# Kernel optimization log

Hardware: AMD Instinct MI355X
Metric: run time of the kernel (lower is better)

The kernel has to match this reference:

```python
import jax, jax.numpy as jnp
import numpy as np

WS, OWS, NH, C = 16, 24, 6, 192


def setup_inputs() -> dict:
    key = jax.random.key(0)
    ks = jax.random.split(key, 20)
    s = 0.05
    inp = {
        'x': jax.random.normal(ks[0], (2, C, 128, 128), jnp.float32),
        'depth': jax.random.normal(ks[1], (2, C, 128, 128), jnp.float32),
        'rpi': jax.random.randint(ks[2], (WS * WS, OWS * OWS), 0, (WS + OWS - 1) ** 2),
        'norm1_w': jnp.ones((C,), jnp.float32),
        'norm1_b': jnp.zeros((C,), jnp.float32),
        'qkv_w': jax.random.normal(ks[3], (C, 3 * C), jnp.float32) * s,
        'qkv_b': jax.random.normal(ks[4], (3 * C,), jnp.float32) * s,
        'dproj_w': jax.random.normal(ks[5], (C, C), jnp.float32) * s,
        'dproj_b': jax.random.normal(ks[6], (C,), jnp.float32) * s,
        'rpb_table': jax.random.normal(ks[7], ((WS + OWS - 1) ** 2, NH), jnp.float32) * 0.02,
        'proj_w': jax.random.normal(ks[8], (C, C), jnp.float32) * s,
        'proj_b': jax.random.normal(ks[9], (C,), jnp.float32) * s,
        'norm2_w': jnp.ones((C,), jnp.float32),
        'norm2_b': jnp.zeros((C,), jnp.float32),
        'fc1_w': jax.random.normal(ks[10], (C, 2 * C), jnp.float32) * s,
        'fc1_b': jax.random.normal(ks[11], (2 * C,), jnp.float32) * s,
        'fc2_w': jax.random.normal(ks[12], (2 * C, C), jnp.float32) * s,
        'fc2_b': jax.random.normal(ks[13], (C,), jnp.float32) * s,
    }
    return inp


def _ln(t, g, b):
    mu = t.mean(-1, keepdims=True)
    var = ((t - mu) ** 2).mean(-1, keepdims=True)
    return (t - mu) / jnp.sqrt(var + 1e-5) * g + b


def reference(x, depth, rpi, norm1_w, norm1_b, qkv_w, qkv_b, dproj_w, dproj_b,
              rpb_table, proj_w, proj_b, norm2_w, norm2_b, fc1_w, fc1_b, fc2_w, fc2_b):
    b, c, h, w = x.shape
    d = c // NH
    scale = d ** -0.5
    pad = (OWS - WS) // 2
    nh, nw = h // WS, w // WS

    xf = jnp.transpose(x, (0, 2, 3, 1))  # b h w c
    qkv = _ln(xf, norm1_w, norm1_b) @ qkv_w + qkv_b  # b h w 3c
    k, v = qkv[..., c:2 * c], qkv[..., 2 * c:]
    # depth_proj is a 1x1 conv == per-pixel linear
    q = jnp.einsum('bhwi,oi->bhwo', jnp.transpose(depth, (0, 2, 3, 1)), dproj_w) + dproj_b

    # non-overlapping query windows
    qw = q.reshape(b, nh, WS, nw, WS, c).transpose(0, 1, 3, 2, 4, 5).reshape(-1, WS * WS, c)

    # overlapping KV windows (unfold: kernel OWS, stride WS, pad (OWS-WS)//2)
    kv = jnp.concatenate([k, v], axis=-1)  # b h w 2c
    kvp = jnp.pad(kv, ((0, 0), (pad, pad), (pad, pad), (0, 0)))
    hh = (jnp.arange(nh) * WS)[:, None] + jnp.arange(OWS)[None]  # [nh, OWS]
    ww = (jnp.arange(nw) * WS)[:, None] + jnp.arange(OWS)[None]  # [nw, OWS]
    patches = kvp[:, hh[:, None, :, None], ww[None, :, None, :], :]  # b nh nw OWS OWS 2c
    patches = patches.reshape(-1, OWS * OWS, 2 * c)
    kw, vw = patches[..., :c], patches[..., c:]

    B, nq, n = qw.shape[0], WS * WS, OWS * OWS
    qh = qw.reshape(B, nq, NH, d).transpose(0, 2, 1, 3) * scale
    kh = kw.reshape(B, n, NH, d).transpose(0, 2, 1, 3)
    vh = vw.reshape(B, n, NH, d).transpose(0, 2, 1, 3)

    attn = jnp.einsum('bhqd,bhkd->bhqk', qh, kh)
    bias = rpb_table[rpi.reshape(-1)].reshape(nq, n, NH).transpose(2, 0, 1)  # H nq n
    attn = jax.nn.softmax(attn + bias[None], axis=-1)
    out = jnp.einsum('bhqk,bhkd->bhqd', attn, vh).transpose(0, 2, 1, 3).reshape(B, nq, c)

    out = out.reshape(b, nh, nw, WS, WS, c).transpose(0, 1, 3, 2, 4, 5).reshape(b, h, w, c)
    out = out @ proj_w + proj_b + xf  # residual
    y = out + (jax.nn.gelu(_ln(out, norm2_w, norm2_b) @ fc1_w + fc1_b, approximate=False) @ fc2_w + fc2_b)
    return jnp.transpose(y, (0, 3, 1, 2))
```

## Files before the change

### kernel.cpp

```cpp
#include <hip/hip_runtime.h>
#include <math.h>

typedef __attribute__((ext_vector_type(8))) short s16x8;
typedef __attribute__((ext_vector_type(4))) short s16x4;
typedef __attribute__((ext_vector_type(4))) float f32x4;

#define DEV __device__ __forceinline__

DEV float b2f(unsigned short u){ unsigned int x = ((unsigned int)u)<<16u; return __builtin_bit_cast(float,x); }
DEV unsigned short f2b(float f){
  unsigned int x = __builtin_bit_cast(unsigned int,f);
  x += 0x7fffu + ((x>>16)&1u);
  return (unsigned short)(x>>16);
}
DEV unsigned int pk_bf16(float lo, float hi){
  unsigned int r;
  asm("v_cvt_pk_bf16_f32 %0, %1, %2" : "=v"(r) : "v"(lo), "v"(hi));
  return r;
}
DEV float ex2(float x){
  float r;
  asm("v_exp_f32 %0, %1" : "=v"(r) : "v"(x));
  return r;
}
DEV float rcpf(float x){
  float r;
  asm("v_rcp_f32 %0, %1" : "=v"(r) : "v"(x));
  return r;
}
#define LOG2E 1.4426950408889634f

__global__ __launch_bounds__(256) void prep_all(
    const float* __restrict__ x, const float* __restrict__ depth,
    const float* __restrict__ g, const float* __restrict__ be,
    const float* __restrict__ qkvw, const float* __restrict__ dprojw,
    const float* __restrict__ projw, const float* __restrict__ fc1w,
    const float* __restrict__ fc2w, const int* __restrict__ rpi,
    const float* __restrict__ rpb,
    unsigned short* xn, unsigned short* xf, unsigned short* dn,
    unsigned short* kvw, unsigned short* dpw, unsigned short* pjw,
    unsigned short* f1w, unsigned short* f2w, unsigned short* bt){
  __shared__ float t[64][193];
  __shared__ float ps[4][64], pq[4][64];
  __shared__ float mu_s[64], rs_s[64];
  int tid = threadIdx.x;
  int bid = blockIdx.x;
  if(bid >= 512){
    int i = (bid - 512)*256 + tid;
    if(i < 73728){
      int n = i/192, k = i - n*192;
      kvw[i] = f2b(qkvw[k*576 + 192 + n]);
    } else if(i < 110592){
      int j = i - 73728;
      dpw[j] = f2b(dprojw[j]);
    } else if(i < 147456){
      int j = i - 110592; int n = j/192, k = j - n*192;
      pjw[j] = f2b(projw[k*192 + n]);
    } else if(i < 221184){
      int j = i - 147456; int n = j/192, k = j - n*192;
      f1w[j] = f2b(fc1w[k*384 + n]);
    } else if(i < 294912){
      int j = i - 221184; int n = j/384, k = j - n*384;
      f2w[j] = f2b(fc2w[k*192 + n]);
    } else {
      int j = i - 294912;
      int h = j/147456; int rr = j - h*147456;
      int kk = rr >> 8; int q = rr & 255;
      int step = kk >> 5, within = kk & 31;
      int lg = within >> 3, p4r = within & 7;
      bt[h*147456 + step*8192 + lg*2048 + q*8 + p4r] =
          f2b(rpb[rpi[q*576 + kk]*6 + h] * LOG2E);
    }
    return;
  }
  long tokbase = (long)bid * 64;
  int b = (int)(tokbase >> 14); int hw = (int)(tokbase & 16383);
  const float* xb = x + ((long)b*192)*16384 + hw;
  int tok = tid & 63, cpart = tid >> 6;
  for(int c = cpart; c < 192; c += 4) t[tok][c] = xb[(long)c*16384 + tok];
  __syncthreads();
  float s = 0.f, q = 0.f;
  #pragma unroll 4
  for(int i = 0; i < 48; i++){ float v = t[tok][cpart*48 + i]; s += v; q += v*v; }
  ps[cpart][tok] = s; pq[cpart][tok] = q;
  __syncthreads();
  if(tid < 64){
    float ss = ps[0][tid]+ps[1][tid]+ps[2][tid]+ps[3][tid];
    float qq = pq[0][tid]+pq[1][tid]+pq[2][tid]+pq[3][tid];
    float mu = ss * (1.f/192.f);
    float var = qq * (1.f/192.f) - mu*mu;
    mu_s[tid] = mu; rs_s[tid] = 1.f/sqrtf(var + 1e-5f);
  }
  __syncthreads();
  long obase = tokbase * 192;
  for(int u = tid; u < 64*192; u += 256){
    int tk = u / 192, ch = u - tk*192;
    float v = t[tk][ch];
    xf[obase + u] = f2b(v);
    xn[obase + u] = f2b((v - mu_s[tk]) * rs_s[tk] * g[ch] + be[ch]);
  }
  __syncthreads();
  const float* db = depth + ((long)b*192)*16384 + hw;
  for(int c = cpart; c < 192; c += 4) t[tok][c] = db[(long)c*16384 + tok];
  __syncthreads();
  for(int u = tid; u < 64*192; u += 256){
    int tk = u / 192, ch = u - tk*192;
    dn[obase + u] = f2b(t[tk][ch]);
  }
}

DEV void gemm_body(const unsigned short* __restrict__ A, const unsigned short* __restrict__ W,
                   const float* __restrict__ bias, const unsigned short* __restrict__ resb,
                   const float* __restrict__ resf, void* outp, int K, int N, int flags, int bid,
                   unsigned short* smem, int tid){
  unsigned short* Al = smem;
  unsigned short* Bl = smem + 9216;
  int lane = tid & 63, wv = tid >> 6;
  int wm = wv >> 1, wn = wv & 1, l15 = lane & 15, lg = lane >> 4;
  int X = bid & 7, j = bid >> 3;
  int mb = X + 8*(j & 31);
  int nb = j >> 5;
  long rowbase = (long)mb * 128;
  int colbase = nb * 64;
  f32x4 acc[4][2];
  #pragma unroll
  for(int m=0;m<4;m++)
    #pragma unroll
    for(int n=0;n<2;n++) acc[m][n] = (f32x4){0.f,0.f,0.f,0.f};
  int nk = K >> 6;
  for(int kt = 0; kt < nk; kt++){
    int k0 = kt*64;
    #pragma unroll
    for(int i = 0; i < 4; i++){
      int u = i*256 + tid; int r = u >> 3, c = u & 7;
      *(s16x8*)(Al + r*72 + c*8) = *(const s16x8*)(A + (rowbase + r)*(long)K + k0 + c*8);
    }
    #pragma unroll
    for(int i = 0; i < 2; i++){
      int u = i*256 + tid; int r = u >> 3, c = u & 7;
      *(s16x8*)(Bl + r*72 + c*8) = *(const s16x8*)(W + (long)(colbase + r)*K + k0 + c*8);
    }
    __syncthreads();
    #pragma unroll
    for(int kk = 0; kk < 64; kk += 32){
      s16x8 af[4], bf[2];
      #pragma unroll
      for(int m = 0; m < 4; m++) af[m] = *(const s16x8*)(Al + (wm*64 + m*16 + l15)*72 + kk + lg*8);
      #pragma unroll
      for(int n = 0; n < 2; n++) bf[n] = *(const s16x8*)(Bl + (wn*32 + n*16 + l15)*72 + kk + lg*8);
      #pragma unroll
      for(int m = 0; m < 4; m++)
        #pragma unroll
        for(int n = 0; n < 2; n++)
          acc[m][n] = __builtin_amdgcn_mfma_f32_16x16x32_bf16(af[m], bf[n], acc[m][n], 0, 0, 0);
    }
    __syncthreads();
  }
  if(flags & 8){
    float vloc[2][4][4];
    #pragma unroll
    for(int n = 0; n < 2; n++){
      int colg = colbase + wn*32 + n*16 + l15;
      float bs = bias[colg];
      #pragma unroll
      for(int m = 0; m < 4; m++){
        long rowg = rowbase + wm*64 + m*16 + lg*4;
        #pragma unroll
        for(int r = 0; r < 4; r++){
          long idx = (rowg + r)*(long)N + colg;
          vloc[n][m][r] = acc[m][n][r] + bs + resf[idx];
        }
      }
    }
    float* T = (float*)smem;
    #pragma unroll
    for(int n = 0; n < 2; n++){
      int chl = wn*32 + n*16 + l15;
      #pragma unroll
      for(int m = 0; m < 4; m++){
        int tl = wm*64 + m*16 + lg*4;
        #pragma unroll
        for(int r = 0; r < 4; r++) T[chl*132 + tl + r] = vloc[n][m][r];
      }
    }
    __syncthreads();
    int bb = (int)(rowbase >> 14), hw0 = (int)(rowbase & 16383);
    float* op = (float*)outp;
    for(int u = tid; u < 8192; u += 256){
      int chn = u >> 7, t2 = u & 127;
      op[((long)bb*192 + colbase + chn)*16384 + hw0 + t2] = T[chn*132 + t2];
    }
    return;
  }
  if(flags & 2){
    float vloc[2][4][4];
    #pragma unroll
    for(int n = 0; n < 2; n++){
      int colg = colbase + wn*32 + n*16 + l15;
      float bs = bias[colg];
      #pragma unroll
      for(int m = 0; m < 4; m++){
        long rowg = rowbase + wm*64 + m*16 + lg*4;
        #pragma unroll
        for(int r = 0; r < 4; r++){
          long idx = (rowg + r)*(long)N + colg;
          vloc[n][m][r] = acc[m][n][r] + bs + b2f(resb[idx]);
        }
      }
    }
    float* T = (float*)smem;
    #pragma unroll
    for(int n = 0; n < 2; n++){
      int colg_l = wn*32 + n*16 + l15;
      #pragma unroll
      for(int m = 0; m < 4; m++){
        int rowl = wm*64 + m*16 + lg*4;
        #pragma unroll
        for(int r = 0; r < 4; r++) T[(rowl + r)*68 + colg_l] = vloc[n][m][r];
      }
    }
    __syncthreads();
    float* op = (float*)outp;
    #pragma unroll
    for(int i = 0; i < 8; i++){
      int u = i*256 + tid;
      int row = u >> 4, c4 = u & 15;
      *(f32x4*)(op + (rowbase + row)*(long)N + colbase + c4*4) = *(const f32x4*)(T + row*68 + c4*4);
    }
    return;
  }
  unsigned short* Ct = smem;
  #pragma unroll
  for(int n = 0; n < 2; n++){
    int colg_l = wn*32 + n*16 + l15;
    float bs = bias[colbase + colg_l];
    #pragma unroll
    for(int m = 0; m < 4; m++){
      int rowl = wm*64 + m*16 + lg*4;
      #pragma unroll
      for(int r = 0; r < 4; r++){
        float v = acc[m][n][r] + bs;
        if(flags & 1){
          float x2 = v*v;
          float u2 = -2.3021174f - 0.10294418f*x2;
          float sg = ex2(v*u2);
          v = v * rcpf(1.f + sg);
        }
        if(flags & 4) v *= (0.17677669529663687f * LOG2E);
        Ct[(rowl + r)*72 + colg_l] = f2b(v);
      }
    }
  }
  __syncthreads();
  unsigned short* op = (unsigned short*)outp;
  #pragma unroll
  for(int i = 0; i < 4; i++){
    int u = i*256 + tid;
    int tok = u >> 3, c8 = u & 7;
    *(s16x8*)(op + (rowbase + tok)*(long)N + colbase + c8*8) = *(const s16x8*)(Ct + tok*72 + c8*8);
  }
}

__global__ __launch_bounds__(256) void gemm_kvq(
    const unsigned short* __restrict__ xn, const unsigned short* __restrict__ dn,
    const unsigned short* __restrict__ kvw, const unsigned short* __restrict__ dpw,
    const float* __restrict__ kvb, const float* __restrict__ dpb,
    unsigned short* kv, unsigned short* qm){
  extern __shared__ unsigned short Bl[];
  int bid = blockIdx.x, tid = threadIdx.x;
  if(bid < 1536) gemm_body(xn, kvw, kvb, nullptr, nullptr, kv, 192, 384, 0, bid, Bl, tid);
  else           gemm_body(dn, dpw, dpb, nullptr, nullptr, qm, 192, 192, 4, bid - 1536, Bl, tid);
}

__global__ __launch_bounds__(256) void gemm2(
    const unsigned short* __restrict__ A, const unsigned short* __restrict__ W,
    const float* __restrict__ bias, const unsigned short* __restrict__ resb,
    const float* __restrict__ resf, void* outp, int K, int N, int flags){
  extern __shared__ unsigned short Bl[];
  gemm_body(A, W, bias, resb, resf, outp, K, N, flags, blockIdx.x, Bl, threadIdx.x);
}

__global__ __launch_bounds__(512, 6) void attn_k(
    const unsigned short* __restrict__ qmat, const unsigned short* __restrict__ kvmat,
    const unsigned short* __restrict__ bt, unsigned short* __restrict__ omat){
  __shared__ unsigned short Kl[192*40];
  __shared__ unsigned short Vl[32*202];
  int tid = threadIdx.x, lane = tid & 63, wv = tid >> 6;
  int l15 = lane & 15, lg = lane >> 4;
  int bid = blockIdx.x;
  int X = bid & 7, j0 = bid >> 3;
  int win = X + 8*(j0 & 15);
  int h = j0 >> 4;
  int b = win >> 6, wi = (win >> 3) & 7, wj = win & 7;
  int qbase = wv*32;

  s16x8 qb[2];
  #pragma unroll
  for(int nt = 0; nt < 2; nt++){
    int q = qbase + nt*16 + l15;
    long tok = (long)b*16384 + (wi*16 + (q>>4))*128 + wj*16 + (q&15);
    qb[nt] = *(const s16x8*)(qmat + tok*192 + h*32 + lg*8);
  }
  const unsigned short* bq[2];
  #pragma unroll
  for(int nt = 0; nt < 2; nt++)
    bq[nt] = bt + h*147456 + lg*2048 + (qbase + nt*16 + l15)*8;

  float l_run[2] = {0.f, 0.f};
  f32x4 oacc[2][2];
  #pragma unroll
  for(int mtd=0;mtd<2;mtd++)
    #pragma unroll
    for(int nt=0;nt<2;nt++) oacc[mtd][nt] = (f32x4){0.f,0.f,0.f,0.f};

  for(int ch = 0; ch < 3; ch++){
    __syncthreads();
    #pragma unroll
    for(int i = 0; i < 3; i++){
      int u = i*512 + tid;
      int p = u >> 3, w8 = u & 7;
      int isV = w8 >> 2, c = w8 & 3;
      int gp = ch*192 + p; int ii = gp / 24, jc = gp - ii*24;
      int gr = wi*16 - 4 + ii, gc = wj*16 - 4 + jc;
      bool ok = (gr >= 0) && (gr < 128) && (gc >= 0) && (gc < 128);
      s16x8 v = (s16x8){0,0,0,0,0,0,0,0};
      if(ok){
        long tok = (long)b*16384 + gr*128 + gc;
        v = *(const s16x8*)(kvmat + tok*384 + isV*192 + h*32 + c*8);
      }
      if(isV == 0){
        int pl = p & 31;
        int srow = (p & ~31) + ((pl & 4) << 2) + ((pl >> 3) << 2) + (pl & 3);
        *(s16x8*)(Kl + srow*40 + c*8) = v;
      } else {
        #pragma unroll
        for(int j2 = 0; j2 < 8; j2++) Vl[(c*8 + j2)*202 + p] = (unsigned short)v[j2];
      }
    }
    __syncthreads();
    #pragma unroll 1
    for(int kt = 0; kt < 6; kt++){
      int kb = kt*32;
      int step = ch*6 + kt;
      s16x8 ka[2];
      #pragma unroll
      for(int mt = 0; mt < 2; mt++) ka[mt] = *(const s16x8*)(Kl + (kb + mt*16 + l15)*40 + lg*8);
      f32x4 zf = (f32x4){0.f,0.f,0.f,0.f};
      f32x4 s[2][2];
      #pragma unroll
      for(int mt = 0; mt < 2; mt++)
        #pragma unroll
        for(int nt = 0; nt < 2; nt++)
          s[mt][nt] = __builtin_amdgcn_mfma_f32_16x16x32_bf16(ka[mt], qb[nt], zf, 0, 0, 0);
      #pragma unroll
      for(int nt = 0; nt < 2; nt++){
        s16x8 bv = *(const s16x8*)(bq[nt] + step*8192);
        #pragma unroll
        for(int mt = 0; mt < 2; mt++)
          #pragma unroll
          for(int r = 0; r < 4; r++) s[mt][nt][r] += b2f((unsigned short)bv[mt*4 + r]);
      }
      s16x8 pb[2];
      #pragma unroll
      for(int nt = 0; nt < 2; nt++){
        float p0 = ex2(s[0][nt][0]);
        float p1 = ex2(s[0][nt][1]);
        float p2 = ex2(s[0][nt][2]);
        float p3 = ex2(s[0][nt][3]);
        float p4 = ex2(s[1][nt][0]);
        float p5 = ex2(s[1][nt][1]);
        float p6 = ex2(s[1][nt][2]);
        float p7 = ex2(s[1][nt][3]);
        l_run[nt] += ((p0+p1)+(p2+p3)) + ((p4+p5)+(p6+p7));
        unsigned int w[4];
        w[0] = pk_bf16(p0, p1); w[1] = pk_bf16(p2, p3);
        w[2] = pk_bf16(p4, p5); w[3] = pk_bf16(p6, p7);
        pb[nt] = __builtin_bit_cast(s16x8, w);
      }
      s16x8 va[2];
      #pragma unroll
      for(int mtd = 0; mtd < 2; mtd++) va[mtd] = *(const s16x8*)(Vl + (mtd*16 + l15)*202 + kb + lg*8);
      #pragma unroll
      for(int mtd = 0; mtd < 2; mtd++)
        #pragma unroll
        for(int nt = 0; nt < 2; nt++)
          oacc[mtd][nt] = __builtin_amdgcn_mfma_f32_16x16x32_bf16(va[mtd], pb[nt], oacc[mtd][nt], 0, 0, 0);
    }
  }
  #pragma unroll
  for(int nt = 0; nt < 2; nt++){
    float l = l_run[nt];
    l += __shfl_xor(l, 16);
    l += __shfl_xor(l, 32);
    float inv = 1.f / l;
    int q = qbase + nt*16 + l15;
    long tok = (long)b*16384 + (wi*16 + (q>>4))*128 + wj*16 + (q&15);
    #pragma unroll
    for(int mtd = 0; mtd < 2; mtd++){
      s16x4 o;
      #pragma unroll
      for(int r = 0; r < 4; r++) o[r] = (short)f2b(oacc[mtd][nt][r] * inv);
      *(s16x4*)(omat + tok*192 + h*32 + mtd*16 + lg*4) = o;
    }
  }
}

__global__ __launch_bounds__(256) void ln2_k(
    const float* __restrict__ in, const float* __restrict__ g,
    const float* __restrict__ be, unsigned short* __restrict__ out){
  int tid = threadIdx.x;
  long tok = (long)blockIdx.x*64 + (tid >> 2);
  int cpart = tid & 3;
  const float* ip = in + tok*192 + cpart*48;
  f32x4 v[12];
  float s = 0.f, q = 0.f;
  #pragma unroll
  for(int i = 0; i < 12; i++){
    v[i] = *(const f32x4*)(ip + i*4);
    #pragma unroll
    for(int r = 0; r < 4; r++){ s += v[i][r]; q += v[i][r]*v[i][r]; }
  }
  s += __shfl_xor(s, 1); s += __shfl_xor(s, 2);
  q += __shfl_xor(q, 1); q += __shfl_xor(q, 2);
  float mu = s * (1.f/192.f);
  float var = q * (1.f/192.f) - mu*mu;
  float rs = 1.f/sqrtf(var + 1e-5f);
  unsigned short* op = out + tok*192 + cpart*48;
  const float* gp = g + cpart*48;
  const float* bp = be + cpart*48;
  #pragma unroll
  for(int i = 0; i < 12; i++){
    f32x4 g4 = *(const f32x4*)(gp + i*4);
    f32x4 b4 = *(const f32x4*)(bp + i*4);
    float o0 = (v[i][0] - mu)*rs*g4[0] + b4[0];
    float o1 = (v[i][1] - mu)*rs*g4[1] + b4[1];
    float o2 = (v[i][2] - mu)*rs*g4[2] + b4[2];
    float o3 = (v[i][3] - mu)*rs*g4[3] + b4[3];
    uint2 pk;
    pk.x = pk_bf16(o0, o1);
    pk.y = pk_bf16(o2, o3);
    *(uint2*)(op + i*4) = pk;
  }
}

extern "C" void kernel_launch(void* const* d_in, const int* in_sizes, int n_in,
                              void* d_out, int out_size, void* d_ws, size_t ws_size,
                              hipStream_t stream) {
  const float* x     = (const float*)d_in[0];
  const float* depth = (const float*)d_in[1];
  const int*   rpi   = (const int*)d_in[2];
  const float* n1w   = (const float*)d_in[3];
  const float* n1b   = (const float*)d_in[4];
  const float* qkvw  = (const float*)d_in[5];
  const float* qkvb  = (const float*)d_in[6];
  const float* dprjw = (const float*)d_in[7];
  const float* dprjb = (const float*)d_in[8];
  const float* rpb   = (const float*)d_in[9];
  const float* prjw  = (const float*)d_in[10];
  const float* prjb  = (const float*)d_in[11];
  const float* n2w   = (const float*)d_in[12];
  const float* n2b   = (const float*)d_in[13];
  const float* fc1w  = (const float*)d_in[14];
  const float* fc1b  = (const float*)d_in[15];
  const float* fc2w  = (const float*)d_in[16];
  const float* fc2b  = (const float*)d_in[17];

  char* ws = (char*)d_ws;
  unsigned short* xn  = (unsigned short*)(ws + 0);
  unsigned short* dn  = (unsigned short*)(ws + 12582912);
  unsigned short* xf  = (unsigned short*)(ws + 25165824);
  unsigned short* kv  = (unsigned short*)(ws + 37748736);
  unsigned short* h1  = (unsigned short*)(ws + 37748736);
  unsigned short* qm  = (unsigned short*)(ws + 62914560);
  float*          r2  = (float*)(ws + 75497472);
  unsigned short* om  = (unsigned short*)(ws + 100663296);
  unsigned short* n2  = (unsigned short*)(ws + 100663296);
  unsigned short* kvw = (unsigned short*)(ws + 113246208);
  unsigned short* dpw = (unsigned short*)(ws + 113393664);
  unsigned short* pjw = (unsigned short*)(ws + 113467392);
  unsigned short* f1w = (unsigned short*)(ws + 113541120);
  unsigned short* f2w = (unsigned short*)(ws + 113688576);
  unsigned short* bt  = (unsigned short*)(ws + 113836032);

  prep_all<<<5120, 256, 0, stream>>>(x, depth, n1w, n1b, qkvw, dprjw, prjw, fc1w, fc2w,
                                     rpi, rpb, xn, xf, dn, kvw, dpw, pjw, f1w, f2w, bt);
  gemm_kvq<<<2304, 256, 27648, stream>>>(xn, dn, kvw, dpw, qkvb + 192, dprjb, kv, qm);
  attn_k<<<768, 512, 0, stream>>>(qm, kv, bt, om);
  gemm2<<<768, 256, 34816, stream>>>(om, pjw, prjb, xf, nullptr, r2, 192, 192, 2);
  ln2_k<<<512, 256, 0, stream>>>(r2, n2w, n2b, n2);
  gemm2<<<1536, 256, 27648, stream>>>(n2, f1w, fc1b, nullptr, nullptr, h1, 192, 384, 1);
  gemm2<<<768, 256, 33792, stream>>>(h1, f2w, fc2b, nullptr, r2, d_out, 384, 192, 8);
}
```

Measured before the change: 134.1 us.

## Store post-attention residual in bf16 and vectorize bias-table prep

The residual stream after the projection GEMM is now written in bf16 through the generic bf16 epilogue with a residual add, instead of a separate fp32 epilogue. LN2 and the final fc2 residual read it as bf16, which halves that buffer's traffic in three kernels. Separately, the relative-position bias table build now has each thread gather 8 entries and issue one vector store, rather than one scalar store per thread, which cuts the prep grid size. Rounding the residual to bf16 adds error to both the LN2 input and the final output's residual term.

```diff
diff --git a/kernel.cpp b/kernel.cpp
--- a/kernel.cpp
+++ b/kernel.cpp
@@ -45,6 +45,19 @@
   __shared__ float mu_s[64], rs_s[64];
   int tid = threadIdx.x;
   int bid = blockIdx.x;
+  if(bid >= 1664){
+    int t2 = (bid - 1664)*256 + tid;
+    int d72 = t2 / 72;
+    int kk8 = t2 - d72*72;
+    int q = d72 & 255;
+    int h = d72 >> 8;
+    const int* rp = rpi + q*576 + kk8*8;
+    unsigned short o[8];
+    #pragma unroll
+    for(int u = 0; u < 8; u++) o[u] = f2b(rpb[rp[u]*6 + h] * LOG2E);
+    *(s16x8*)(bt + h*147456 + (kk8>>2)*8192 + (kk8&3)*2048 + q*8) = *(const s16x8*)o;
+    return;
+  }
   if(bid >= 512){
     int i = (bid - 512)*256 + tid;
     if(i < 73728){
@@ -59,17 +72,9 @@
     } else if(i < 221184){
       int j = i - 147456; int n = j/192, k = j - n*192;
       f1w[j] = f2b(fc1w[k*384 + n]);
-    } else if(i < 294912){
+    } else {
       int j = i - 221184; int n = j/384, k = j - n*384;
       f2w[j] = f2b(fc2w[k*192 + n]);
-    } else {
-      int j = i - 294912;
-      int h = j/147456; int rr = j - h*147456;
-      int kk = rr >> 8; int q = rr & 255;
-      int step = kk >> 5, within = kk & 31;
-      int lg = within >> 3, p4r = within & 7;
-      bt[h*147456 + step*8192 + lg*2048 + q*8 + p4r] =
-          f2b(rpb[rpi[q*576 + kk]*6 + h] * LOG2E);
     }
     return;
   }
@@ -111,7 +116,7 @@
 
 DEV void gemm_body(const unsigned short* __restrict__ A, const unsigned short* __restrict__ W,
                    const float* __restrict__ bias, const unsigned short* __restrict__ resb,
-                   const float* __restrict__ resf, void* outp, int K, int N, int flags, int bid,
+                   void* outp, int K, int N, int flags, int bid,
                    unsigned short* smem, int tid){
   unsigned short* Al = smem;
   unsigned short* Bl = smem + 9216;
@@ -168,7 +173,7 @@
         #pragma unroll
         for(int r = 0; r < 4; r++){
           long idx = (rowg + r)*(long)N + colg;
-          vloc[n][m][r] = acc[m][n][r] + bs + resf[idx];
+          vloc[n][m][r] = acc[m][n][r] + bs + b2f(resb[idx]);
         }
       }
     }
@@ -189,43 +194,6 @@
     for(int u = tid; u < 8192; u += 256){
       int chn = u >> 7, t2 = u & 127;
       op[((long)bb*192 + colbase + chn)*16384 + hw0 + t2] = T[chn*132 + t2];
-    }
-    return;
-  }
-  if(flags & 2){
-    float vloc[2][4][4];
-    #pragma unroll
-    for(int n = 0; n < 2; n++){
-      int colg = colbase + wn*32 + n*16 + l15;
-      float bs = bias[colg];
-      #pragma unroll
-      for(int m = 0; m < 4; m++){
-        long rowg = rowbase + wm*64 + m*16 + lg*4;
-        #pragma unroll
-        for(int r = 0; r < 4; r++){
-          long idx = (rowg + r)*(long)N + colg;
-          vloc[n][m][r] = acc[m][n][r] + bs + b2f(resb[idx]);
-        }
-      }
-    }
-    float* T = (float*)smem;
-    #pragma unroll
-    for(int n = 0; n < 2; n++){
-      int colg_l = wn*32 + n*16 + l15;
-      #pragma unroll
-      for(int m = 0; m < 4; m++){
-        int rowl = wm*64 + m*16 + lg*4;
-        #pragma unroll
-        for(int r = 0; r < 4; r++) T[(rowl + r)*68 + colg_l] = vloc[n][m][r];
-      }
-    }
-    __syncthreads();
-    float* op = (float*)outp;
-    #pragma unroll
-    for(int i = 0; i < 8; i++){
-      int u = i*256 + tid;
-      int row = u >> 4, c4 = u & 15;
-      *(f32x4*)(op + (rowbase + row)*(long)N + colbase + c4*4) = *(const f32x4*)(T + row*68 + c4*4);
     }
     return;
   }
@@ -247,6 +215,10 @@
           v = v * rcpf(1.f + sg);
         }
         if(flags & 4) v *= (0.17677669529663687f * LOG2E);
+        if(flags & 16){
+          long idx = (rowbase + rowl + r)*(long)N + colbase + colg_l;
+          v += b2f(resb[idx]);
+        }
         Ct[(rowl + r)*72 + colg_l] = f2b(v);
       }
     }
@@ -268,16 +240,16 @@
     unsigned short* kv, unsigned short* qm){
   extern __shared__ unsigned short Bl[];
   int bid = blockIdx.x, tid = threadIdx.x;
-  if(bid < 1536) gemm_body(xn, kvw, kvb, nullptr, nullptr, kv, 192, 384, 0, bid, Bl, tid);
-  else           gemm_body(dn, dpw, dpb, nullptr, nullptr, qm, 192, 192, 4, bid - 1536, Bl, tid);
+  if(bid < 1536) gemm_body(xn, kvw, kvb, nullptr, kv, 192, 384, 0, bid, Bl, tid);
+  else           gemm_body(dn, dpw, dpb, nullptr, qm, 192, 192, 4, bid - 1536, Bl, tid);
 }
 
 __global__ __launch_bounds__(256) void gemm2(
     const unsigned short* __restrict__ A, const unsigned short* __restrict__ W,
     const float* __restrict__ bias, const unsigned short* __restrict__ resb,
-    const float* __restrict__ resf, void* outp, int K, int N, int flags){
+    void* outp, int K, int N, int flags){
   extern __shared__ unsigned short Bl[];
-  gemm_body(A, W, bias, resb, resf, outp, K, N, flags, blockIdx.x, Bl, threadIdx.x);
+  gemm_body(A, W, bias, resb, outp, K, N, flags, blockIdx.x, Bl, threadIdx.x);
 }
 
 __global__ __launch_bounds__(512, 6) void attn_k(
@@ -406,19 +378,22 @@
 }
 
 __global__ __launch_bounds__(256) void ln2_k(
-    const float* __restrict__ in, const float* __restrict__ g,
+    const unsigned short* __restrict__ in, const float* __restrict__ g,
     const float* __restrict__ be, unsigned short* __restrict__ out){
   int tid = threadIdx.x;
   long tok = (long)blockIdx.x*64 + (tid >> 2);
   int cpart = tid & 3;
-  const float* ip = in + tok*192 + cpart*48;
-  f32x4 v[12];
+  const unsigned short* ip = in + tok*192 + cpart*48;
+  float v[48];
   float s = 0.f, q = 0.f;
   #pragma unroll
-  for(int i = 0; i < 12; i++){
-    v[i] = *(const f32x4*)(ip + i*4);
-    #pragma unroll
-    for(int r = 0; r < 4; r++){ s += v[i][r]; q += v[i][r]*v[i][r]; }
+  for(int i = 0; i < 6; i++){
+    s16x8 h8 = *(const s16x8*)(ip + i*8);
+    #pragma unroll
+    for(int r = 0; r < 8; r++){
+      float f = b2f((unsigned short)h8[r]);
+      v[i*8+r] = f; s += f; q += f*f;
+    }
   }
   s += __shfl_xor(s, 1); s += __shfl_xor(s, 2);
   q += __shfl_xor(q, 1); q += __shfl_xor(q, 2);
@@ -429,17 +404,15 @@
   const float* gp = g + cpart*48;
   const float* bp = be + cpart*48;
   #pragma unroll
-  for(int i = 0; i < 12; i++){
-    f32x4 g4 = *(const f32x4*)(gp + i*4);
-    f32x4 b4 = *(const f32x4*)(bp + i*4);
-    float o0 = (v[i][0] - mu)*rs*g4[0] + b4[0];
-    float o1 = (v[i][1] - mu)*rs*g4[1] + b4[1];
-    float o2 = (v[i][2] - mu)*rs*g4[2] + b4[2];
-    float o3 = (v[i][3] - mu)*rs*g4[3] + b4[3];
-    uint2 pk;
-    pk.x = pk_bf16(o0, o1);
-    pk.y = pk_bf16(o2, o3);
-    *(uint2*)(op + i*4) = pk;
+  for(int i = 0; i < 6; i++){
+    unsigned int w[4];
+    #pragma unroll
+    for(int pr = 0; pr < 4; pr++){
+      float o0 = (v[i*8+pr*2]   - mu)*rs*gp[i*8+pr*2]   + bp[i*8+pr*2];
+      float o1 = (v[i*8+pr*2+1] - mu)*rs*gp[i*8+pr*2+1] + bp[i*8+pr*2+1];
+      w[pr] = pk_bf16(o0, o1);
+    }
+    *(s16x8*)(op + i*8) = __builtin_bit_cast(s16x8, w);
   }
 }
 
@@ -472,7 +445,7 @@
   unsigned short* kv  = (unsigned short*)(ws + 37748736);
   unsigned short* h1  = (unsigned short*)(ws + 37748736);
   unsigned short* qm  = (unsigned short*)(ws + 62914560);
-  float*          r2  = (float*)(ws + 75497472);
+  unsigned short* r2b = (unsigned short*)(ws + 75497472);
   unsigned short* om  = (unsigned short*)(ws + 100663296);
   unsigned short* n2  = (unsigned short*)(ws + 100663296);
   unsigned short* kvw = (unsigned short*)(ws + 113246208);
@@ -482,12 +455,12 @@
   unsigned short* f2w = (unsigned short*)(ws + 113688576);
   unsigned short* bt  = (unsigned short*)(ws + 113836032);
 
-  prep_all<<<5120, 256, 0, stream>>>(x, depth, n1w, n1b, qkvw, dprjw, prjw, fc1w, fc2w,
+  prep_all<<<2096, 256, 0, stream>>>(x, depth, n1w, n1b, qkvw, dprjw, prjw, fc1w, fc2w,
                                      rpi, rpb, xn, xf, dn, kvw, dpw, pjw, f1w, f2w, bt);
   gemm_kvq<<<2304, 256, 27648, stream>>>(xn, dn, kvw, dpw, qkvb + 192, dprjb, kv, qm);
   attn_k<<<768, 512, 0, stream>>>(qm, kv, bt, om);
-  gemm2<<<768, 256, 34816, stream>>>(om, pjw, prjb, xf, nullptr, r2, 192, 192, 2);
-  ln2_k<<<512, 256, 0, stream>>>(r2, n2w, n2b, n2);
-  gemm2<<<1536, 256, 27648, stream>>>(n2, f1w, fc1b, nullptr, nullptr, h1, 192, 384, 1);
-  gemm2<<<768, 256, 33792, stream>>>(h1, f2w, fc2b, nullptr, r2, d_out, 384, 192, 8);
-}
+  gemm2<<<768, 256, 27648, stream>>>(om, pjw, prjb, xf, r2b, 192, 192, 16);
+  ln2_k<<<512, 256, 0, stream>>>(r2b, n2w, n2b, n2);
+  gemm2<<<1536, 256, 27648, stream>>>(n2, f1w, fc1b, nullptr, h1, 192, 384, 1);
+  gemm2<<<768, 256, 33792, stream>>>(h1, f2w, fc2b, r2b, d_out, 384, 192, 8);
+}
```

Measured after the change: 138.6 us. 1.03x slower.
